# Performance work log

Hardware: AMD Instinct MI355X
Metric: run time of the kernel (lower is better)

The kernel has to match this reference:

```python
import jax, jax.numpy as jnp
import numpy as np

THRESH = 0.3
LENS = 0.3
DECAY = 0.5
IN_SIZE = 8
PIXELS = 784
T = PIXELS // IN_SIZE  # 98 timesteps
FC = (512, 512, 512)
OUT_SIZE = 10
SKIP = (4, 8, 16)
BATCH = 512


def _make_mask(dim, cycle, t_steps):
    # faithful to create_mask: base pattern 1 at t % cycle == 0, rolled per neuron
    base = np.array([1 if t % cycle == 0 else 0 for t in range(t_steps)], dtype=np.int32)
    return np.stack([np.roll(base, n) for n in range(dim)])  # [dim, T]


def _slice_idx():
    # faithful to the original slicing (incl. the time_window-based boundary condition)
    starts = [s * IN_SIZE if s * IN_SIZE < T - IN_SIZE else PIXELS - IN_SIZE for s in range(T)]
    return np.asarray([list(range(st, st + IN_SIZE)) for st in starts], dtype=np.int32)  # [T, 8]


def setup_inputs() -> dict:
    key = jax.random.key(0)
    ks = jax.random.split(key, 5)

    def lin(k, fan_in, fan_out):
        bound = 1.0 / np.sqrt(fan_in)
        kw, kb = jax.random.split(k)
        w = jax.random.uniform(kw, (fan_out, fan_in), jnp.float32, -bound, bound)
        b = jax.random.uniform(kb, (fan_out,), jnp.float32, -bound, bound)
        return w, b

    w1, b1 = lin(ks[0], IN_SIZE, FC[0])
    w2, b2 = lin(ks[1], FC[0], FC[1])
    w3, b3 = lin(ks[2], FC[1], FC[2])
    w4, b4 = lin(ks[3], FC[2], OUT_SIZE)
    x = jax.random.uniform(ks[4], (BATCH, PIXELS), jnp.float32)
    m1 = jnp.asarray(_make_mask(FC[0], SKIP[0], T))
    m2 = jnp.asarray(_make_mask(FC[1], SKIP[1], T))
    m3 = jnp.asarray(_make_mask(FC[2], SKIP[2], T))
    return {"input": x, "w1": w1, "b1": b1, "w2": w2, "b2": b2,
            "w3": w3, "b3": b3, "w4": w4, "b4": b4,
            "m1": m1, "m2": m2, "m3": m3}


def act_fun(x):
    # ActFun.forward: hard threshold spike
    return (x > THRESH).astype(x.dtype)


def reference(input, w1, b1, w2, b2, w3, b3, w4, b4, m1, m2, m3):
    N = input.shape[0]
    idx = jnp.asarray(_slice_idx())                      # [T, 8]
    xs = jnp.transpose(input[:, idx], (1, 0, 2))         # [T, N, 8]
    mk1 = m1.T.astype(input.dtype)                       # [T, FC0]
    mk2 = m2.T.astype(input.dtype)
    mk3 = m3.T.astype(input.dtype)

    def upd(w, b, x, mem, spike, mk):
        # mem_update_skip_woDecay
        new = mem * DECAY * (1.0 - spike) + x @ w.T + b
        mem2 = jnp.where(mk == 0.0, mem, new)
        sp = act_fun(mem2) * mk
        return mem2, sp

    z = lambda d: jnp.zeros((N, d), input.dtype)
    carry0 = (z(FC[0]), z(FC[0]), z(FC[1]), z(FC[1]), z(FC[2]), z(FC[2]), jnp.zeros((N, OUT_SIZE), input.dtype))

    def step(carry, inp):
        h1m, h1s, h2m, h2s, h3m, h3s, osum = carry
        x, k1, k2, k3 = inp
        h1m, h1s = upd(w1, b1, x, h1m, h1s, k1)
        h2m, h2s = upd(w2, b2, h1s, h2m, h2s, k2)
        h3m, h3s = upd(w3, b3, h2s, h3m, h3s, k3)
        osum = osum + h3s @ w4.T + b4
        return (h1m, h1s, h2m, h2s, h3m, h3s, osum), None

    carry, _ = jax.lax.scan(step, carry0, (xs, mk1, mk2, mk3))
    return carry[-1] / T
```

## Files before the change

kernel.cpp:

```cpp
#include <hip/hip_runtime.h>
#include <cstddef>
#include <cstdint>

#define T_STEPS 98
#define CAP1 136
#define CAP2 72
#define CAP3 40

#define BLOBF   14848
#define OB_CNT  0
#define OB_ACT1 4
#define OB_ACT2 140
#define OB_ACT3 212
#define OB_B1   252
#define OB_B2   388
#define OB_B3   460
#define OB_W4   500
#define OB_W1T  980
#define OB_W3   2068
#define OB_W2   4948

__device__ __forceinline__ void gld16(const float* g, float* l) {
  __builtin_amdgcn_global_load_lds(
      (const __attribute__((address_space(1))) float*)g,
      (__attribute__((address_space(3))) float*)l, 16, 0, 0);
}

__global__ __launch_bounds__(512) void k_setup(
    const float* __restrict__ w1, const float* __restrict__ b1,
    const float* __restrict__ w2, const float* __restrict__ b2,
    const float* __restrict__ w3, const float* __restrict__ b3,
    const float* __restrict__ w4,
    const int* __restrict__ m1, const int* __restrict__ m2, const int* __restrict__ m3,
    float* __restrict__ wsF)
{
  const int t = blockIdx.x;
  const int tid = threadIdx.x;
  const int lane = tid & 63, wv = tid >> 6;
  __shared__ int wtot[8], wbase[8];
  __shared__ int sa1[CAP1], sa2[CAP2], sa3[CAP3];
  __shared__ int scnt[3];
  const int* ms[3] = {m1, m2, m3};
  int* sas[3] = {sa1, sa2, sa3};
  const int caps[3] = {CAP1, CAP2, CAP3};

  for (int L = 0; L < 3; ++L) {
    bool p = (ms[L][tid*T_STEPS + t] != 0);
    unsigned long long mk = __ballot(p);
    if (lane == 0) wtot[wv] = __popcll(mk);
    __syncthreads();
    if (tid == 0) {
      int s = 0;
      for (int q = 0; q < 8; ++q) { wbase[q] = s; s += wtot[q]; }
      scnt[L] = (s > caps[L]) ? caps[L] : s;
    }
    __syncthreads();
    int pos = wbase[wv] + __popcll(mk & ((1ull << lane) - 1ull));
    if (p && pos < caps[L]) sas[L][pos] = tid;
    __syncthreads();
  }
  const int c1 = scnt[0], c2 = scnt[1], c3 = scnt[2];

  float* blob = wsF + (size_t)t * BLOBF;
  int* blobI = (int*)blob;
  if (tid == 0) { blobI[OB_CNT] = c1; blobI[OB_CNT+1] = c2; blobI[OB_CNT+2] = c3; blobI[OB_CNT+3] = 0; }
  for (int i = tid; i < c1; i += 512) { blobI[OB_ACT1 + i] = sa1[i]; blob[OB_B1 + i] = b1[sa1[i]]; }
  for (int l = tid; l < c2; l += 512) { blobI[OB_ACT2 + l] = sa2[l]; blob[OB_B2 + l] = b2[sa2[l]]; }
  for (int l = tid; l < c3; l += 512) { blobI[OB_ACT3 + l] = sa3[l]; blob[OB_B3 + l] = b3[sa3[l]]; }

  for (int q = tid; q < c1*8; q += 512) {
    int i = q >> 3, j = q & 7;
    blob[OB_W1T + j*CAP1 + i] = w1[sa1[i]*8 + j];
  }
  for (int q = tid; q < c1*CAP2; q += 512) {
    int i = q / CAP2, l = q - i*CAP2;
    if (l < c2) blob[OB_W2 + i*CAP2 + l] = w2[(size_t)sa2[l]*512 + sa1[i]];
  }
  for (int q = tid; q < c2*CAP3; q += 512) {
    int i = q / CAP3, l = q - i*CAP3;
    if (l < c3) blob[OB_W3 + i*CAP3 + l] = w3[(size_t)sa3[l]*512 + sa2[i]];
  }
  for (int q = tid; q < c3*12; q += 512) {
    int i = q / 12, o = q - i*12;
    if (o < 10) blob[OB_W4 + i*12 + o] = w4[(size_t)o*512 + sa3[i]];
  }
}

__global__ __launch_bounds__(256) void k_main(
    const float* __restrict__ x, const float* __restrict__ b4,
    const float* __restrict__ wsF, float* __restrict__ out)
{
  const int lane = threadIdx.x & 63;
  const int w = threadIdx.x >> 6;
  const int elem = blockIdx.x * 4 + w;

  __shared__ float s_blob[2][BLOBF];
  __shared__ float s_mem[4][1536];
  __shared__ alignas(8) unsigned char s_f1[4][CAP1];
  __shared__ alignas(8) unsigned char s_f2[4][CAP2];
  __shared__ alignas(8) unsigned char s_f3[4][CAP3];

  for (int i = lane; i < 1536; i += 64) s_mem[w][i] = 0.f;

  const float* xrow = x + (size_t)elem * 784;
  float4 xA = *(const float4*)(xrow);
  float4 xB = *(const float4*)(xrow + 4);

  for (int i = w; i < 58; i += 4)
    gld16(wsF + (size_t)i*256 + lane*4, &s_blob[0][i*256]);

  float osum = 0.f;
  __syncthreads();

  for (int t = 0; t < T_STEPS; ++t) {
    const float* B = s_blob[t & 1];
    const int* Bi = (const int*)B;

    if (t < T_STEPS - 1) {
      const float* src = wsF + (size_t)(t+1) * BLOBF;
      float* dst = (float*)s_blob[(t+1) & 1];
      for (int i = w; i < 58; i += 4)
        gld16(src + (size_t)i*256 + lane*4, dst + i*256);
    }

    const int c1 = Bi[OB_CNT], c2 = Bi[OB_CNT+1], c3 = Bi[OB_CNT+2];
    const float xv0 = xA.x, xv1 = xA.y, xv2 = xA.z, xv3 = xA.w;
    const float xv4 = xB.x, xv5 = xB.y, xv6 = xB.z, xv7 = xB.w;
    if (t < 11)       { xA = *(const float4*)(xrow + 8*(t+1)); xB = *(const float4*)(xrow + 8*(t+1) + 4); }
    else if (t == 11) { xA = *(const float4*)(xrow + 776);     xB = *(const float4*)(xrow + 780); }

    int nf1 = 0;
    for (int c0 = 0; c0 < c1; c0 += 64) {
      const int i = c0 + lane;
      bool p = false;
      if (i < c1) {
        const int k = Bi[OB_ACT1 + i];
        const float* w1t = B + OB_W1T + i;
        const float dot = w1t[0]*xv0     + w1t[136]*xv1   + w1t[272]*xv2   + w1t[408]*xv3
                        + w1t[544]*xv4   + w1t[680]*xv5   + w1t[816]*xv6   + w1t[952]*xv7;
        const float nv = s_mem[w][k]*0.5f + dot + B[OB_B1 + i];
        s_mem[w][k] = nv;
        p = nv > 0.3f;
      }
      const unsigned long long mk = __ballot(p);
      if (p) s_f1[w][nf1 + __popcll(mk & ((1ull << lane) - 1ull))] = (unsigned char)i;
      nf1 += __popcll(mk);
    }

    int nf2 = 0;
    {
      const float* w2b = B + OB_W2 + lane;
      float a0=0.f,a1=0.f,a2=0.f,a3=0.f,a4=0.f,a5=0.f,a6=0.f,a7=0.f;
      int f = 0;
      for (; f + 8 <= nf1; f += 8) {
        const uint64_t pk = *(const uint64_t*)&s_f1[w][f];
        const int i0 = (int)(pk      ) & 255, i1 = (int)(pk >>  8) & 255;
        const int i2 = (int)(pk >> 16) & 255, i3 = (int)(pk >> 24) & 255;
        const int i4 = (int)(pk >> 32) & 255, i5 = (int)(pk >> 40) & 255;
        const int i6 = (int)(pk >> 48) & 255, i7 = (int)(pk >> 56);
        a0 += w2b[i0*CAP2]; a1 += w2b[i1*CAP2]; a2 += w2b[i2*CAP2]; a3 += w2b[i3*CAP2];
        a4 += w2b[i4*CAP2]; a5 += w2b[i5*CAP2]; a6 += w2b[i6*CAP2]; a7 += w2b[i7*CAP2];
      }
      for (; f < nf1; ++f) a0 += w2b[(int)s_f1[w][f]*CAP2];
      const float accLo = ((a0+a1)+(a2+a3)) + ((a4+a5)+(a6+a7));
      {
        bool p = false;
        if (lane < c2) {
          const int k2 = Bi[OB_ACT2 + lane];
          const float nv = s_mem[w][512 + k2]*0.5f + accLo + B[OB_B2 + lane];
          s_mem[w][512 + k2] = nv;
          p = nv > 0.3f;
        }
        const unsigned long long mk = __ballot(p);
        if (p) s_f2[w][__popcll(mk & ((1ull << lane) - 1ull))] = (unsigned char)lane;
        nf2 = __popcll(mk);
      }
      {
        const int g = lane >> 4;
        const int l = 64 + g;
        float a = 0.f;
        for (int f2 = lane & 15; f2 < nf1; f2 += 16)
          a += B[OB_W2 + (int)s_f1[w][f2]*CAP2 + l];
        a += __shfl_xor(a, 1); a += __shfl_xor(a, 2);
        a += __shfl_xor(a, 4); a += __shfl_xor(a, 8);
        bool p = false;
        if ((lane & 15) == 0 && l < c2) {
          const int k2 = Bi[OB_ACT2 + l];
          const float nv = s_mem[w][512 + k2]*0.5f + a + B[OB_B2 + l];
          s_mem[w][512 + k2] = nv;
          p = nv > 0.3f;
        }
        const unsigned long long mk = __ballot(p);
        if (p) s_f2[w][nf2 + __popcll(mk & ((1ull << lane) - 1ull))] = (unsigned char)l;
        nf2 += __popcll(mk);
      }
    }

    int nf3 = 0;
    {
      bool p = false;
      if (lane < c3) {
        const float* w3b = B + OB_W3 + lane;
        float a0=0.f,a1=0.f,a2=0.f,a3=0.f;
        int f = 0;
        for (; f + 8 <= nf2; f += 8) {
          const uint64_t pk = *(const uint64_t*)&s_f2[w][f];
          const int i0 = (int)(pk      ) & 255, i1 = (int)(pk >>  8) & 255;
          const int i2 = (int)(pk >> 16) & 255, i3 = (int)(pk >> 24) & 255;
          const int i4 = (int)(pk >> 32) & 255, i5 = (int)(pk >> 40) & 255;
          const int i6 = (int)(pk >> 48) & 255, i7 = (int)(pk >> 56);
          a0 += w3b[i0*CAP3]; a1 += w3b[i1*CAP3]; a2 += w3b[i2*CAP3]; a3 += w3b[i3*CAP3];
          a0 += w3b[i4*CAP3]; a1 += w3b[i5*CAP3]; a2 += w3b[i6*CAP3]; a3 += w3b[i7*CAP3];
        }
        for (; f < nf2; ++f) a0 += w3b[(int)s_f2[w][f]*CAP3];
        const float acc = (a0+a1) + (a2+a3);
        const int k3 = Bi[OB_ACT3 + lane];
        const float nv = s_mem[w][1024 + k3]*0.5f + acc + B[OB_B3 + lane];
        s_mem[w][1024 + k3] = nv;
        p = nv > 0.3f;
      }
      const unsigned long long mk = __ballot(p);
      if (p) s_f3[w][__popcll(mk & ((1ull << lane) - 1ull))] = (unsigned char)lane;
      nf3 = __popcll(mk);
    }

    if (lane < 10) {
      float o0 = 0.f, o1 = 0.f;
      int f = 0;
      for (; f + 2 <= nf3; f += 2) {
        o0 += B[OB_W4 + (int)s_f3[w][f]  *12 + lane];
        o1 += B[OB_W4 + (int)s_f3[w][f+1]*12 + lane];
      }
      if (f < nf3) o0 += B[OB_W4 + (int)s_f3[w][f]*12 + lane];
      osum += o0 + o1;
    }

    __syncthreads();
  }

  if (lane < 10) out[(size_t)elem*10 + lane] = osum / 98.f + b4[lane];
}

extern "C" void kernel_launch(void* const* d_in, const int* in_sizes, int n_in,
                              void* d_out, int out_size, void* d_ws, size_t ws_size,
                              hipStream_t stream)
{
  const float* x  = (const float*)d_in[0];
  const float* w1 = (const float*)d_in[1];
  const float* b1 = (const float*)d_in[2];
  const float* w2 = (const float*)d_in[3];
  const float* b2 = (const float*)d_in[4];
  const float* w3 = (const float*)d_in[5];
  const float* b3 = (const float*)d_in[6];
  const float* w4 = (const float*)d_in[7];
  const float* b4 = (const float*)d_in[8];
  const int* m1 = (const int*)d_in[9];
  const int* m2 = (const int*)d_in[10];
  const int* m3 = (const int*)d_in[11];
  float* wsF = (float*)d_ws;
  float* out = (float*)d_out;

  hipLaunchKernelGGL(k_setup, dim3(T_STEPS), dim3(512), 0, stream,
                     w1, b1, w2, b2, w3, b3, w4, m1, m2, m3, wsF);
  hipLaunchKernelGGL(k_main, dim3(128), dim3(256), 0, stream, x, b4, wsF, out);
}
```

Measured before the change: 375.0 us.

## Replace spike index lists with ballot bitmasks and transposed vectorized weight rows

Instead of compacting fired-neuron indices into LDS byte lists and gathering weights by index, each layer keeps the ballot masks in registers. Each lane then walks a transposed, zero-padded weight row with float4 loads, selecting terms by mask bits. Membrane storage gets padding (k + k/8) to reduce bank conflicts, and the blob is padded to fixed capacities so the loops have fixed trip counts. The trade is dense work proportional to capacity rather than spike count, plus a slightly larger per-step blob transfer and a row stride that may cause LDS bank conflicts.

```diff
diff --git a/kernel.cpp b/kernel.cpp
--- a/kernel.cpp
+++ b/kernel.cpp
@@ -7,24 +7,27 @@
 #define CAP2 72
 #define CAP3 40
 
-#define BLOBF   14848
-#define OB_CNT  0
-#define OB_ACT1 4
-#define OB_ACT2 140
-#define OB_ACT3 212
-#define OB_B1   252
-#define OB_B2   388
-#define OB_B3   460
-#define OB_W4   500
-#define OB_W1T  980
-#define OB_W3   2068
-#define OB_W2   4948
+#define OB_CNT   0
+#define OB_ACT1  4
+#define OB_ACT2  196
+#define OB_ACT3  268
+#define OB_B1    308
+#define OB_B2    500
+#define OB_B3    572
+#define OB_W4T   612
+#define OB_W1T   1052
+#define OB_W3T   2588
+#define OB_W2T   5628
+#define BLOBF    15360
+#define NCHUNK   60
 
 __device__ __forceinline__ void gld16(const float* g, float* l) {
   __builtin_amdgcn_global_load_lds(
       (const __attribute__((address_space(1))) float*)g,
       (__attribute__((address_space(3))) float*)l, 16, 0, 0);
 }
+
+__device__ __forceinline__ int midx(int k) { return k + (k >> 3); }
 
 __global__ __launch_bounds__(512) void k_setup(
     const float* __restrict__ w1, const float* __restrict__ b1,
@@ -64,25 +67,34 @@
   float* blob = wsF + (size_t)t * BLOBF;
   int* blobI = (int*)blob;
   if (tid == 0) { blobI[OB_CNT] = c1; blobI[OB_CNT+1] = c2; blobI[OB_CNT+2] = c3; blobI[OB_CNT+3] = 0; }
-  for (int i = tid; i < c1; i += 512) { blobI[OB_ACT1 + i] = sa1[i]; blob[OB_B1 + i] = b1[sa1[i]]; }
-  for (int l = tid; l < c2; l += 512) { blobI[OB_ACT2 + l] = sa2[l]; blob[OB_B2 + l] = b2[sa2[l]]; }
-  for (int l = tid; l < c3; l += 512) { blobI[OB_ACT3 + l] = sa3[l]; blob[OB_B3 + l] = b3[sa3[l]]; }
-
-  for (int q = tid; q < c1*8; q += 512) {
-    int i = q >> 3, j = q & 7;
-    blob[OB_W1T + j*CAP1 + i] = w1[sa1[i]*8 + j];
-  }
-  for (int q = tid; q < c1*CAP2; q += 512) {
-    int i = q / CAP2, l = q - i*CAP2;
-    if (l < c2) blob[OB_W2 + i*CAP2 + l] = w2[(size_t)sa2[l]*512 + sa1[i]];
-  }
-  for (int q = tid; q < c2*CAP3; q += 512) {
-    int i = q / CAP3, l = q - i*CAP3;
-    if (l < c3) blob[OB_W3 + i*CAP3 + l] = w3[(size_t)sa3[l]*512 + sa2[i]];
-  }
-  for (int q = tid; q < c3*12; q += 512) {
-    int i = q / 12, o = q - i*12;
-    if (o < 10) blob[OB_W4 + i*12 + o] = w4[(size_t)o*512 + sa3[i]];
+
+  for (int i = tid; i < 192; i += 512) {
+    blobI[OB_ACT1 + i] = (i < c1) ? sa1[i] : 0;
+    blob[OB_B1 + i]    = (i < c1) ? b1[sa1[i]] : 0.f;
+  }
+  for (int l = tid; l < 72; l += 512) {
+    blobI[OB_ACT2 + l] = (l < c2) ? sa2[l] : 0;
+    blob[OB_B2 + l]    = (l < c2) ? b2[sa2[l]] : 0.f;
+  }
+  for (int l = tid; l < 40; l += 512) {
+    blobI[OB_ACT3 + l] = (l < c3) ? sa3[l] : 0;
+    blob[OB_B3 + l]    = (l < c3) ? b3[sa3[l]] : 0.f;
+  }
+  for (int q = tid; q < 8*192; q += 512) {
+    int j = q / 192, i = q - j*192;
+    blob[OB_W1T + q] = (i < c1) ? w1[sa1[i]*8 + j] : 0.f;
+  }
+  for (int q = tid; q < 10*44; q += 512) {
+    int o = q / 44, i = q - o*44;
+    blob[OB_W4T + q] = (i < c3) ? w4[(size_t)o*512 + sa3[i]] : 0.f;
+  }
+  for (int q = tid; q < 40*76; q += 512) {
+    int l = q / 76, i = q - l*76;
+    blob[OB_W3T + q] = (l < c3 && i < c2) ? w3[(size_t)sa3[l]*512 + sa2[i]] : 0.f;
+  }
+  for (int q = tid; q < 68*140; q += 512) {
+    int l = q / 140, i = q - l*140;
+    blob[OB_W2T + q] = (l < c2 && i < c1) ? w2[(size_t)sa2[l]*512 + sa1[i]] : 0.f;
   }
 }
 
@@ -94,19 +106,16 @@
   const int w = threadIdx.x >> 6;
   const int elem = blockIdx.x * 4 + w;
 
-  __shared__ float s_blob[2][BLOBF];
-  __shared__ float s_mem[4][1536];
-  __shared__ alignas(8) unsigned char s_f1[4][CAP1];
-  __shared__ alignas(8) unsigned char s_f2[4][CAP2];
-  __shared__ alignas(8) unsigned char s_f3[4][CAP3];
-
-  for (int i = lane; i < 1536; i += 64) s_mem[w][i] = 0.f;
+  __shared__ alignas(16) float s_blob[2][BLOBF];
+  __shared__ float s_mem[4][1920];
+
+  for (int i = threadIdx.x; i < 4*1920; i += 256) (&s_mem[0][0])[i] = 0.f;
 
   const float* xrow = x + (size_t)elem * 784;
   float4 xA = *(const float4*)(xrow);
   float4 xB = *(const float4*)(xrow + 4);
 
-  for (int i = w; i < 58; i += 4)
+  for (int i = w; i < NCHUNK; i += 4)
     gld16(wsF + (size_t)i*256 + lane*4, &s_blob[0][i*256]);
 
   float osum = 0.f;
@@ -119,120 +128,156 @@
     if (t < T_STEPS - 1) {
       const float* src = wsF + (size_t)(t+1) * BLOBF;
       float* dst = (float*)s_blob[(t+1) & 1];
-      for (int i = w; i < 58; i += 4)
+      for (int i = w; i < NCHUNK; i += 4)
         gld16(src + (size_t)i*256 + lane*4, dst + i*256);
     }
 
     const int c1 = Bi[OB_CNT], c2 = Bi[OB_CNT+1], c3 = Bi[OB_CNT+2];
-    const float xv0 = xA.x, xv1 = xA.y, xv2 = xA.z, xv3 = xA.w;
-    const float xv4 = xB.x, xv5 = xB.y, xv6 = xB.z, xv7 = xB.w;
+    const float xv0=xA.x, xv1=xA.y, xv2=xA.z, xv3=xA.w;
+    const float xv4=xB.x, xv5=xB.y, xv6=xB.z, xv7=xB.w;
     if (t < 11)       { xA = *(const float4*)(xrow + 8*(t+1)); xB = *(const float4*)(xrow + 8*(t+1) + 4); }
     else if (t == 11) { xA = *(const float4*)(xrow + 776);     xB = *(const float4*)(xrow + 780); }
 
-    int nf1 = 0;
-    for (int c0 = 0; c0 < c1; c0 += 64) {
-      const int i = c0 + lane;
-      bool p = false;
-      if (i < c1) {
-        const int k = Bi[OB_ACT1 + i];
-        const float* w1t = B + OB_W1T + i;
-        const float dot = w1t[0]*xv0     + w1t[136]*xv1   + w1t[272]*xv2   + w1t[408]*xv3
-                        + w1t[544]*xv4   + w1t[680]*xv5   + w1t[816]*xv6   + w1t[952]*xv7;
-        const float nv = s_mem[w][k]*0.5f + dot + B[OB_B1 + i];
-        s_mem[w][k] = nv;
-        p = nv > 0.3f;
-      }
-      const unsigned long long mk = __ballot(p);
-      if (p) s_f1[w][nf1 + __popcll(mk & ((1ull << lane) - 1ull))] = (unsigned char)i;
-      nf1 += __popcll(mk);
-    }
-
-    int nf2 = 0;
+    float* mem = s_mem[w];
+
+    uint64_t m1w0 = 0, m1w1 = 0, m1w2 = 0;
+    #pragma unroll
+    for (int c = 0; c < 3; ++c) {
+      const int i = c*64 + lane;
+      const int k = Bi[OB_ACT1 + i];
+      const float* w1t = B + OB_W1T + i;
+      const float dot = w1t[0]*xv0    + w1t[192]*xv1  + w1t[384]*xv2  + w1t[576]*xv3
+                      + w1t[768]*xv4  + w1t[960]*xv5  + w1t[1152]*xv6 + w1t[1344]*xv7;
+      const int mi = midx(k);
+      const float nv = mem[mi]*0.5f + dot + B[OB_B1 + i];
+      const bool act = (i < c1);
+      if (act) mem[mi] = nv;
+      const uint64_t mk = __ballot(act && (nv > 0.3f));
+      if (c == 0) m1w0 = mk; else if (c == 1) m1w1 = mk; else m1w2 = mk;
+    }
+
+    uint64_t m2a, m2b;
     {
-      const float* w2b = B + OB_W2 + lane;
-      float a0=0.f,a1=0.f,a2=0.f,a3=0.f,a4=0.f,a5=0.f,a6=0.f,a7=0.f;
-      int f = 0;
-      for (; f + 8 <= nf1; f += 8) {
-        const uint64_t pk = *(const uint64_t*)&s_f1[w][f];
-        const int i0 = (int)(pk      ) & 255, i1 = (int)(pk >>  8) & 255;
-        const int i2 = (int)(pk >> 16) & 255, i3 = (int)(pk >> 24) & 255;
-        const int i4 = (int)(pk >> 32) & 255, i5 = (int)(pk >> 40) & 255;
-        const int i6 = (int)(pk >> 48) & 255, i7 = (int)(pk >> 56);
-        a0 += w2b[i0*CAP2]; a1 += w2b[i1*CAP2]; a2 += w2b[i2*CAP2]; a3 += w2b[i3*CAP2];
-        a4 += w2b[i4*CAP2]; a5 += w2b[i5*CAP2]; a6 += w2b[i6*CAP2]; a7 += w2b[i7*CAP2];
-      }
-      for (; f < nf1; ++f) a0 += w2b[(int)s_f1[w][f]*CAP2];
-      const float accLo = ((a0+a1)+(a2+a3)) + ((a4+a5)+(a6+a7));
-      {
-        bool p = false;
-        if (lane < c2) {
-          const int k2 = Bi[OB_ACT2 + lane];
-          const float nv = s_mem[w][512 + k2]*0.5f + accLo + B[OB_B2 + lane];
-          s_mem[w][512 + k2] = nv;
-          p = nv > 0.3f;
-        }
-        const unsigned long long mk = __ballot(p);
-        if (p) s_f2[w][__popcll(mk & ((1ull << lane) - 1ull))] = (unsigned char)lane;
-        nf2 = __popcll(mk);
-      }
-      {
-        const int g = lane >> 4;
-        const int l = 64 + g;
-        float a = 0.f;
-        for (int f2 = lane & 15; f2 < nf1; f2 += 16)
-          a += B[OB_W2 + (int)s_f1[w][f2]*CAP2 + l];
-        a += __shfl_xor(a, 1); a += __shfl_xor(a, 2);
-        a += __shfl_xor(a, 4); a += __shfl_xor(a, 8);
-        bool p = false;
-        if ((lane & 15) == 0 && l < c2) {
+      const float* r = B + OB_W2T + lane*140;
+      float a0=0.f, a1=0.f, a2=0.f, a3=0.f;
+      #pragma unroll
+      for (int kq = 0; kq < 16; ++kq) {
+        const float4 v = *(const float4*)(r + kq*4);
+        a0 += ((m1w0 >> (4*kq  )) & 1) ? v.x : 0.f;
+        a1 += ((m1w0 >> (4*kq+1)) & 1) ? v.y : 0.f;
+        a2 += ((m1w0 >> (4*kq+2)) & 1) ? v.z : 0.f;
+        a3 += ((m1w0 >> (4*kq+3)) & 1) ? v.w : 0.f;
+      }
+      #pragma unroll
+      for (int kq = 0; kq < 16; ++kq) {
+        const float4 v = *(const float4*)(r + 64 + kq*4);
+        a0 += ((m1w1 >> (4*kq  )) & 1) ? v.x : 0.f;
+        a1 += ((m1w1 >> (4*kq+1)) & 1) ? v.y : 0.f;
+        a2 += ((m1w1 >> (4*kq+2)) & 1) ? v.z : 0.f;
+        a3 += ((m1w1 >> (4*kq+3)) & 1) ? v.w : 0.f;
+      }
+      #pragma unroll
+      for (int kq = 0; kq < 2; ++kq) {
+        const float4 v = *(const float4*)(r + 128 + kq*4);
+        a0 += ((m1w2 >> (4*kq  )) & 1) ? v.x : 0.f;
+        a1 += ((m1w2 >> (4*kq+1)) & 1) ? v.y : 0.f;
+        a2 += ((m1w2 >> (4*kq+2)) & 1) ? v.z : 0.f;
+        a3 += ((m1w2 >> (4*kq+3)) & 1) ? v.w : 0.f;
+      }
+      const float acc = (a0+a1) + (a2+a3);
+      const int k2 = Bi[OB_ACT2 + lane];
+      const int mi = 640 + midx(k2);
+      const float nv = mem[mi]*0.5f + acc + B[OB_B2 + lane];
+      mem[mi] = nv;
+      m2a = __ballot(nv > 0.3f);
+    }
+    {
+      bool pt = false;
+      if (lane < 4) {
+        const float* r = B + OB_W2T + (64 + lane)*140;
+        float a0=0.f, a1=0.f, a2=0.f, a3=0.f;
+        #pragma unroll
+        for (int kq = 0; kq < 16; ++kq) {
+          const float4 v = *(const float4*)(r + kq*4);
+          a0 += ((m1w0 >> (4*kq  )) & 1) ? v.x : 0.f;
+          a1 += ((m1w0 >> (4*kq+1)) & 1) ? v.y : 0.f;
+          a2 += ((m1w0 >> (4*kq+2)) & 1) ? v.z : 0.f;
+          a3 += ((m1w0 >> (4*kq+3)) & 1) ? v.w : 0.f;
+        }
+        #pragma unroll
+        for (int kq = 0; kq < 16; ++kq) {
+          const float4 v = *(const float4*)(r + 64 + kq*4);
+          a0 += ((m1w1 >> (4*kq  )) & 1) ? v.x : 0.f;
+          a1 += ((m1w1 >> (4*kq+1)) & 1) ? v.y : 0.f;
+          a2 += ((m1w1 >> (4*kq+2)) & 1) ? v.z : 0.f;
+          a3 += ((m1w1 >> (4*kq+3)) & 1) ? v.w : 0.f;
+        }
+        #pragma unroll
+        for (int kq = 0; kq < 2; ++kq) {
+          const float4 v = *(const float4*)(r + 128 + kq*4);
+          a0 += ((m1w2 >> (4*kq  )) & 1) ? v.x : 0.f;
+          a1 += ((m1w2 >> (4*kq+1)) & 1) ? v.y : 0.f;
+          a2 += ((m1w2 >> (4*kq+2)) & 1) ? v.z : 0.f;
+          a3 += ((m1w2 >> (4*kq+3)) & 1) ? v.w : 0.f;
+        }
+        const float acc = (a0+a1) + (a2+a3);
+        const int l = 64 + lane;
+        if (l < c2) {
           const int k2 = Bi[OB_ACT2 + l];
-          const float nv = s_mem[w][512 + k2]*0.5f + a + B[OB_B2 + l];
-          s_mem[w][512 + k2] = nv;
-          p = nv > 0.3f;
-        }
-        const unsigned long long mk = __ballot(p);
-        if (p) s_f2[w][nf2 + __popcll(mk & ((1ull << lane) - 1ull))] = (unsigned char)l;
-        nf2 += __popcll(mk);
-      }
-    }
-
-    int nf3 = 0;
+          const int mi = 640 + midx(k2);
+          const float nv = mem[mi]*0.5f + acc + B[OB_B2 + l];
+          mem[mi] = nv;
+          pt = nv > 0.3f;
+        }
+      }
+      m2b = __ballot(pt);
+    }
+
+    uint64_t m3;
     {
       bool p = false;
-      if (lane < c3) {
-        const float* w3b = B + OB_W3 + lane;
-        float a0=0.f,a1=0.f,a2=0.f,a3=0.f;
-        int f = 0;
-        for (; f + 8 <= nf2; f += 8) {
-          const uint64_t pk = *(const uint64_t*)&s_f2[w][f];
-          const int i0 = (int)(pk      ) & 255, i1 = (int)(pk >>  8) & 255;
-          const int i2 = (int)(pk >> 16) & 255, i3 = (int)(pk >> 24) & 255;
-          const int i4 = (int)(pk >> 32) & 255, i5 = (int)(pk >> 40) & 255;
-          const int i6 = (int)(pk >> 48) & 255, i7 = (int)(pk >> 56);
-          a0 += w3b[i0*CAP3]; a1 += w3b[i1*CAP3]; a2 += w3b[i2*CAP3]; a3 += w3b[i3*CAP3];
-          a0 += w3b[i4*CAP3]; a1 += w3b[i5*CAP3]; a2 += w3b[i6*CAP3]; a3 += w3b[i7*CAP3];
-        }
-        for (; f < nf2; ++f) a0 += w3b[(int)s_f2[w][f]*CAP3];
+      if (lane < 40) {
+        const float* r = B + OB_W3T + lane*76;
+        float a0=0.f, a1=0.f, a2=0.f, a3=0.f;
+        #pragma unroll
+        for (int kq = 0; kq < 16; ++kq) {
+          const float4 v = *(const float4*)(r + kq*4);
+          a0 += ((m2a >> (4*kq  )) & 1) ? v.x : 0.f;
+          a1 += ((m2a >> (4*kq+1)) & 1) ? v.y : 0.f;
+          a2 += ((m2a >> (4*kq+2)) & 1) ? v.z : 0.f;
+          a3 += ((m2a >> (4*kq+3)) & 1) ? v.w : 0.f;
+        }
+        {
+          const float4 v = *(const float4*)(r + 64);
+          a0 += ( m2b        & 1) ? v.x : 0.f;
+          a1 += ((m2b >> 1)  & 1) ? v.y : 0.f;
+          a2 += ((m2b >> 2)  & 1) ? v.z : 0.f;
+          a3 += ((m2b >> 3)  & 1) ? v.w : 0.f;
+        }
         const float acc = (a0+a1) + (a2+a3);
-        const int k3 = Bi[OB_ACT3 + lane];
-        const float nv = s_mem[w][1024 + k3]*0.5f + acc + B[OB_B3 + lane];
-        s_mem[w][1024 + k3] = nv;
-        p = nv > 0.3f;
-      }
-      const unsigned long long mk = __ballot(p);
-      if (p) s_f3[w][__popcll(mk & ((1ull << lane) - 1ull))] = (unsigned char)lane;
-      nf3 = __popcll(mk);
+        if (lane < c3) {
+          const int k3 = Bi[OB_ACT3 + lane];
+          const int mi = 1280 + midx(k3);
+          const float nv = mem[mi]*0.5f + acc + B[OB_B3 + lane];
+          mem[mi] = nv;
+          p = nv > 0.3f;
+        }
+      }
+      m3 = __ballot(p);
     }
 
     if (lane < 10) {
-      float o0 = 0.f, o1 = 0.f;
-      int f = 0;
-      for (; f + 2 <= nf3; f += 2) {
-        o0 += B[OB_W4 + (int)s_f3[w][f]  *12 + lane];
-        o1 += B[OB_W4 + (int)s_f3[w][f+1]*12 + lane];
-      }
-      if (f < nf3) o0 += B[OB_W4 + (int)s_f3[w][f]*12 + lane];
-      osum += o0 + o1;
+      const float* r = B + OB_W4T + lane*44;
+      float o0=0.f, o1=0.f, o2=0.f, o3=0.f;
+      #pragma unroll
+      for (int kq = 0; kq < 10; ++kq) {
+        const float4 v = *(const float4*)(r + kq*4);
+        o0 += ((m3 >> (4*kq  )) & 1) ? v.x : 0.f;
+        o1 += ((m3 >> (4*kq+1)) & 1) ? v.y : 0.f;
+        o2 += ((m3 >> (4*kq+2)) & 1) ? v.z : 0.f;
+        o3 += ((m3 >> (4*kq+3)) & 1) ? v.w : 0.f;
+      }
+      osum += (o0+o1) + (o2+o3);
     }
 
     __syncthreads();
```

Result: slower. 616.5 us (+64.4%).
